# Kernel optimization log

Hardware: AMD Instinct MI355X
Metric: run time of the kernel (lower is better)

## Reference

```python
import jax, jax.numpy as jnp
import numpy as np

B, F, E, U = 16384, 1024, 8, 512
EH1, EH2 = 1024, 1024
TH1, TH2 = 512, 256
T = 4


def setup_inputs() -> dict:
    key = jax.random.key(0)
    ks = jax.random.split(key, 16)
    s = lambda k, shape: jax.random.normal(k, shape, dtype=jnp.float32) * 0.02
    return {
        "x": jax.random.normal(ks[0], (B, F), dtype=jnp.float32),
        # stacked expert MLP params [E, ...]
        "We1": s(ks[1], (E, F, EH1)), "be1": s(ks[2], (E, EH1)),
        "We2": s(ks[3], (E, EH1, EH2)), "be2": s(ks[4], (E, EH2)),
        "We3": s(ks[5], (E, EH2, U)), "be3": s(ks[6], (E, U)),
        # per-task gates [T, F, E]
        "Wg": jax.random.normal(ks[7], (T, F, E), dtype=jnp.float32),
        # stacked tower params [T, ...]
        "Wt1": s(ks[8], (T, U, TH1)), "bt1": s(ks[9], (T, TH1)),
        "Wt2": s(ks[10], (T, TH1, TH2)), "bt2": s(ks[11], (T, TH2)),
        "Wt3": s(ks[12], (T, TH2, 1)), "bt3": s(ks[13], (T, 1)),
    }


def reference(x, We1, be1, We2, be2, We3, be3, Wg, Wt1, bt1, Wt2, bt2, Wt3, bt3):
    relu = jax.nn.relu
    # experts: all E small MLPs batched as one grouped GEMM chain -> [E, B, U]
    h = relu(jnp.einsum('bf,efh->ebh', x, We1) + be1[:, None, :])
    h = relu(jnp.einsum('ebh,ehk->ebk', h, We2) + be2[:, None, :])
    expert_out = jnp.einsum('ebk,eku->ebu', h, We3) + be3[:, None, :]
    # per-task gates: softmax over expert axis -> [T, B, E]
    gates = jax.nn.softmax(jnp.einsum('bf,tfe->tbe', x, Wg), axis=-1)
    # gate-weighted combine over experts -> [T, B, U]
    ti = jnp.einsum('tbe,ebu->tbu', gates, expert_out)
    # per-task towers -> [T, B, 1]
    g = relu(jnp.einsum('tbu,tuh->tbh', ti, Wt1) + bt1[:, None, :])
    g = relu(jnp.einsum('tbh,thk->tbk', g, Wt2) + bt2[:, None, :])
    out = jnp.einsum('tbk,tko->tbo', g, Wt3) + bt3[:, None, :]
    return out  # [T, B, 1], equivalent to list of per-task [B, 1] outputs
```

## Files before the change

### kernel.cpp

```cpp
#include <hip/hip_runtime.h>
#include <hip/hip_bf16.h>
#include <cstdint>

#define B_ 16384
#define F_ 1024
#define E_ 8
#define U_ 512
#define EH1_ 1024
#define EH2_ 1024
#define TH1_ 512
#define TH2_ 256
#define T_ 4

typedef __attribute__((ext_vector_type(4))) float f32x4;
typedef __attribute__((ext_vector_type(8))) short bf16x8;
typedef __attribute__((ext_vector_type(4))) short s16x4;

__device__ __forceinline__ short f2bf(float f) {
  union { float f; unsigned u; } v; v.f = f;
  unsigned r = v.u + 0x7fffu + ((v.u >> 16) & 1u);
  return (short)(r >> 16);
}
__device__ __forceinline__ float bf2f(short s) {
  union { unsigned u; float f; } v; v.u = ((unsigned)(unsigned short)s) << 16;
  return v.f;
}

__device__ __forceinline__ void gload16(const void* g, void* l) {
  __builtin_amdgcn_global_load_lds(
      (const __attribute__((address_space(1))) void*)g,
      (__attribute__((address_space(3))) void*)l, 16, 0, 0);
}

__global__ __launch_bounds__(256) void conv_dual(const float* __restrict__ in,
                                                 short* __restrict__ ob,
                                                 short* __restrict__ orr, long n) {
  long i = ((long)blockIdx.x * 256 + threadIdx.x) * 8;
  if (i >= n) return;
  const float4* p = (const float4*)(in + i);
  float4 a = p[0], b = p[1];
  float v[8] = {a.x, a.y, a.z, a.w, b.x, b.y, b.z, b.w};
  bf16x8 o, r;
#pragma unroll
  for (int j = 0; j < 8; j++) {
    short s = f2bf(v[j]);
    o[j] = s;
    r[j] = f2bf(v[j] - bf2f(s));
  }
  *(bf16x8*)(ob + i) = o;
  *(bf16x8*)(orr + i) = r;
}

__global__ __launch_bounds__(256) void trans_conv(const float* __restrict__ W,
                                                  short* __restrict__ Wt, int K, int N) {
  __shared__ float tile[32][33];
  const int e = blockIdx.z;
  const int k0 = blockIdx.x * 32, n0 = blockIdx.y * 32;
  const float* We = W + (size_t)e * K * N;
  short* Wte = Wt + (size_t)e * N * K;
  const int tx = threadIdx.x, ty = threadIdx.y;
#pragma unroll
  for (int r = 0; r < 32; r += 8)
    tile[ty + r][tx] = We[(size_t)(k0 + ty + r) * N + (n0 + tx)];
  __syncthreads();
#pragma unroll
  for (int r = 0; r < 32; r += 8)
    Wte[(size_t)(n0 + ty + r) * K + (k0 + tx)] = f2bf(tile[tx][ty + r]);
}

__global__ __launch_bounds__(256) void trans_wg(const float* __restrict__ Wg,
                                                short* __restrict__ Wp,
                                                short* __restrict__ Wr) {
  int idx = blockIdx.x * 256 + threadIdx.x;
  int p = idx >> 10, f = idx & 1023;
  int t = p >> 3, e = p & 7;
  float w = Wg[((size_t)t * F_ + f) * E_ + e];
  short wb = f2bf(w);
  Wp[idx] = wb;
  Wr[idx] = f2bf(w - bf2f(wb));
}

__global__ __launch_bounds__(256) void glogits(const short* __restrict__ xb,
                                               const short* __restrict__ xr,
                                               const short* __restrict__ Wp,
                                               const short* __restrict__ Wr,
                                               float* __restrict__ gates) {
  const int wid = threadIdx.x >> 6, lane = threadIdx.x & 63;
  const int m0 = blockIdx.x * 64 + wid * 16;
  const int fr = lane & 15, kg = (lane >> 4) * 8;
  f32x4 acc[2];
#pragma unroll
  for (int j = 0; j < 2; j++)
#pragma unroll
    for (int r = 0; r < 4; r++) acc[j][r] = 0.f;

  const short* Aterm[3] = {xb, xb, xr};
  const short* Bterm[3] = {Wp, Wr, Wp};
#pragma unroll
  for (int term = 0; term < 3; ++term) {
    const short* A = Aterm[term] + (size_t)(m0 + fr) * F_ + kg;
    const short* Bt0 = Bterm[term] + (size_t)fr * F_ + kg;
    const short* Bt1 = Bterm[term] + (size_t)(16 + fr) * F_ + kg;
    for (int k0 = 0; k0 < F_; k0 += 32) {
      bf16x8 a = *(const bf16x8*)(A + k0);
      bf16x8 b0 = *(const bf16x8*)(Bt0 + k0);
      bf16x8 b1 = *(const bf16x8*)(Bt1 + k0);
      acc[0] = __builtin_amdgcn_mfma_f32_16x16x32_bf16(a, b0, acc[0], 0, 0, 0);
      acc[1] = __builtin_amdgcn_mfma_f32_16x16x32_bf16(a, b1, acc[1], 0, 0, 0);
    }
  }
  const int cc = lane & 15;
#pragma unroll
  for (int j = 0; j < 2; ++j) {
    const int t = j * 2 + (cc >> 3), e = cc & 7;
#pragma unroll
    for (int r = 0; r < 4; ++r) {
      float s = acc[j][r];
      float mx = s;
      mx = fmaxf(mx, __shfl_xor(mx, 1, 64));
      mx = fmaxf(mx, __shfl_xor(mx, 2, 64));
      mx = fmaxf(mx, __shfl_xor(mx, 4, 64));
      float ex = __expf(s - mx);
      float sm = ex;
      sm += __shfl_xor(sm, 1, 64);
      sm += __shfl_xor(sm, 2, 64);
      sm += __shfl_xor(sm, 4, 64);
      const int b = m0 + (lane >> 4) * 4 + r;
      gates[((size_t)t * B_ + b) * E_ + e] = ex / sm;
    }
  }
}

template <int RELU>
__global__ __launch_bounds__(256, 2) void gemm_bt(const short* __restrict__ A0, size_t sA,
                                                  const short* __restrict__ B0, size_t sB,
                                                  const float* __restrict__ bias0, size_t sBias,
                                                  short* __restrict__ C0, size_t sC,
                                                  int M, int N, int K) {
  const int z = blockIdx.z;
  const short* A = A0 + (size_t)z * sA;
  const short* Bt = B0 + (size_t)z * sB;
  const float* bias = bias0 + (size_t)z * sBias;
  short* C = C0 + (size_t)z * sC;

  __shared__ short As[128 * 64];
  __shared__ short Bs[128 * 64];
  const int tid = threadIdx.x;
  const int wid = tid >> 6;
  const int lane = tid & 63;
  const int m0 = blockIdx.x * 128;
  const int n0 = blockIdx.y * 128;
  const int wm = (wid >> 1) * 64;
  const int wn = (wid & 1) * 64;

  f32x4 acc[4][4];
#pragma unroll
  for (int i = 0; i < 4; i++)
#pragma unroll
    for (int j = 0; j < 4; j++)
#pragma unroll
      for (int r = 0; r < 4; r++) acc[i][j][r] = 0.f;

  const int srow8 = lane >> 3;
  const int scolb = (((lane & 7) ^ srow8) << 4);
  const short* aS = A + (size_t)(m0 + wid * 8 + srow8) * K + (scolb >> 1);
  const short* bS = Bt + (size_t)(n0 + wid * 8 + srow8) * K + (scolb >> 1);
  char* Adst = (char*)As + wid * 1024;
  char* Bdst = (char*)Bs + wid * 1024;

  const int fr = lane & 15;
  const int g = lane >> 4;
  const int swzR = (fr & 7) << 4;
  const char* Ard = (const char*)As + (wm + fr) * 128;
  const char* Brd = (const char*)Bs + (wn + fr) * 128;

  for (int k0 = 0; k0 < K; k0 += 64) {
#pragma unroll
    for (int c = 0; c < 4; ++c) {
      gload16(aS + (size_t)c * 32 * K + k0, Adst + c * 4096);
      gload16(bS + (size_t)c * 32 * K + k0, Bdst + c * 4096);
    }
    __syncthreads();
    {
      const int ca = (g * 16) ^ swzR;
      bf16x8 af[4], bfv[4];
#pragma unroll
      for (int i = 0; i < 4; i++) af[i] = *(const bf16x8*)(Ard + i * 2048 + ca);
#pragma unroll
      for (int j = 0; j < 4; j++) bfv[j] = *(const bf16x8*)(Brd + j * 2048 + ca);
      __builtin_amdgcn_s_setprio(1);
#pragma unroll
      for (int i = 0; i < 4; i++)
#pragma unroll
        for (int j = 0; j < 4; j++)
          acc[i][j] = __builtin_amdgcn_mfma_f32_16x16x32_bf16(af[i], bfv[j], acc[i][j], 0, 0, 0);
      __builtin_amdgcn_s_setprio(0);
    }
    {
      const int ca = (64 + g * 16) ^ swzR;
      bf16x8 af[4], bfv[4];
#pragma unroll
      for (int i = 0; i < 4; i++) af[i] = *(const bf16x8*)(Ard + i * 2048 + ca);
#pragma unroll
      for (int j = 0; j < 4; j++) bfv[j] = *(const bf16x8*)(Brd + j * 2048 + ca);
      __builtin_amdgcn_s_setprio(1);
#pragma unroll
      for (int i = 0; i < 4; i++)
#pragma unroll
        for (int j = 0; j < 4; j++)
          acc[i][j] = __builtin_amdgcn_mfma_f32_16x16x32_bf16(af[i], bfv[j], acc[i][j], 0, 0, 0);
      __builtin_amdgcn_s_setprio(0);
    }
    __syncthreads();
  }

  const int cr4 = (lane >> 4) * 4;
  const int cc = lane & 15;
#pragma unroll
  for (int j = 0; j < 4; j++) {
    const int col = n0 + wn + j * 16 + cc;
    const float bv = bias[col];
#pragma unroll
    for (int i = 0; i < 4; i++) {
      const int row = m0 + wm + i * 16 + cr4;
#pragma unroll
      for (int r = 0; r < 4; r++) {
        float v = acc[i][j][r] + bv;
        if (RELU) v = fmaxf(v, 0.f);
        C[(size_t)(row + r) * N + col] = f2bf(v);
      }
    }
  }
}

__global__ __launch_bounds__(256) void combine_kernel(const short* __restrict__ EO,
                                                      const float* __restrict__ gates,
                                                      short* __restrict__ ti,
                                                      int Bc, int b0) {
  const int idx = blockIdx.x * 256 + threadIdx.x;
  const int lb = idx >> 6;
  const int uc = (idx & 63) * 8;
  float acc[T_][8];
#pragma unroll
  for (int t = 0; t < T_; t++)
#pragma unroll
    for (int j = 0; j < 8; j++) acc[t][j] = 0.f;
#pragma unroll
  for (int e = 0; e < E_; e++) {
    bf16x8 v = *(const bf16x8*)&EO[((size_t)e * Bc + lb) * U_ + uc];
    float f[8];
#pragma unroll
    for (int j = 0; j < 8; j++) f[j] = bf2f(v[j]);
#pragma unroll
    for (int t = 0; t < T_; t++) {
      const float g = gates[((size_t)t * B_ + b0 + lb) * E_ + e];
#pragma unroll
      for (int j = 0; j < 8; j++) acc[t][j] += g * f[j];
    }
  }
#pragma unroll
  for (int t = 0; t < T_; t++) {
    bf16x8 o;
#pragma unroll
    for (int j = 0; j < 8; j++) o[j] = f2bf(acc[t][j]);
    *(bf16x8*)&ti[((size_t)t * Bc + lb) * U_ + uc] = o;
  }
}

__global__ __launch_bounds__(256) void tower3_kernel(const short* __restrict__ G2,
                                                     const float* __restrict__ Wt3,
                                                     const float* __restrict__ bt3,
                                                     float* __restrict__ out,
                                                     int bcShift, int b0) {
  const int wid = threadIdx.x >> 6, lane = threadIdx.x & 63;
  const int rowl = blockIdx.x * 4 + wid;
  const int t = rowl >> bcShift;
  const int lb = rowl & ((1 << bcShift) - 1);
  const short* g = G2 + (size_t)rowl * TH2_;
  s16x4 gv = *(const s16x4*)(g + lane * 4);
  float4 wv = *(const float4*)(Wt3 + t * TH2_ + lane * 4);
  float s = bf2f(gv[0]) * wv.x + bf2f(gv[1]) * wv.y + bf2f(gv[2]) * wv.z + bf2f(gv[3]) * wv.w;
#pragma unroll
  for (int off = 32; off; off >>= 1) s += __shfl_xor(s, off, 64);
  if (lane == 0) out[(size_t)t * B_ + b0 + lb] = s + bt3[t];
}

extern "C" void kernel_launch(void* const* d_in, const int* in_sizes, int n_in,
                              void* d_out, int out_size, void* d_ws, size_t ws_size,
                              hipStream_t stream) {
  const float* x   = (const float*)d_in[0];
  const float* We1 = (const float*)d_in[1];
  const float* be1 = (const float*)d_in[2];
  const float* We2 = (const float*)d_in[3];
  const float* be2 = (const float*)d_in[4];
  const float* We3 = (const float*)d_in[5];
  const float* be3 = (const float*)d_in[6];
  const float* Wg  = (const float*)d_in[7];
  const float* Wt1 = (const float*)d_in[8];
  const float* bt1 = (const float*)d_in[9];
  const float* Wt2 = (const float*)d_in[10];
  const float* bt2 = (const float*)d_in[11];
  const float* Wt3 = (const float*)d_in[12];
  const float* bt3 = (const float*)d_in[13];
  float* out = (float*)d_out;
  (void)in_sizes; (void)n_in; (void)out_size;

  char* ws = (char*)d_ws;
  size_t off = 0;
  auto alloc = [&](size_t bytes) {
    char* p = ws + off;
    off += (bytes + 255) & ~(size_t)255;
    return p;
  };
  short* We1b  = (short*)alloc((size_t)E_ * F_ * EH1_ * 2);
  short* We2b  = (short*)alloc((size_t)E_ * EH1_ * EH2_ * 2);
  short* We3b  = (short*)alloc((size_t)E_ * EH2_ * U_ * 2);
  short* Wt1b  = (short*)alloc((size_t)T_ * U_ * TH1_ * 2);
  short* Wt2b  = (short*)alloc((size_t)T_ * TH1_ * TH2_ * 2);
  short* Wgp   = (short*)alloc((size_t)32 * F_ * 2);
  short* Wgr   = (short*)alloc((size_t)32 * F_ * 2);
  float* gates = (float*)alloc((size_t)T_ * B_ * E_ * 4);
  short* xb    = (short*)alloc((size_t)B_ * F_ * 2);
  short* xrb   = (short*)alloc((size_t)B_ * F_ * 2);
  const size_t persist = off;

  int Bc = 16384;
  while (Bc > 256 && persist + (size_t)Bc * 32768 + 65536 > ws_size) Bc >>= 1;
  const int bcShift = __builtin_ctz((unsigned)Bc);

  short* h1 = (short*)alloc((size_t)E_ * Bc * EH1_ * 2);
  short* h2 = (short*)alloc((size_t)E_ * Bc * EH2_ * 2);
  short* EO = h1;
  short* ti = h2;
  short* G1 = h2 + (size_t)Bc * 2048;
  short* G2 = h2 + (size_t)Bc * 4096;

  conv_dual<<<(B_ * F_ / 8 + 255) / 256, 256, 0, stream>>>(x, xb, xrb, (long)B_ * F_);
  dim3 tb(32, 8);
  trans_conv<<<dim3(F_ / 32, EH1_ / 32, E_), tb, 0, stream>>>(We1, We1b, F_, EH1_);
  trans_conv<<<dim3(EH1_ / 32, EH2_ / 32, E_), tb, 0, stream>>>(We2, We2b, EH1_, EH2_);
  trans_conv<<<dim3(EH2_ / 32, U_ / 32, E_), tb, 0, stream>>>(We3, We3b, EH2_, U_);
  trans_conv<<<dim3(U_ / 32, TH1_ / 32, T_), tb, 0, stream>>>(Wt1, Wt1b, U_, TH1_);
  trans_conv<<<dim3(TH1_ / 32, TH2_ / 32, T_), tb, 0, stream>>>(Wt2, Wt2b, TH1_, TH2_);
  trans_wg<<<(32 * F_) / 256, 256, 0, stream>>>(Wg, Wgp, Wgr);

  glogits<<<B_ / 64, 256, 0, stream>>>(xb, xrb, Wgp, Wgr, gates);

  for (int b0 = 0; b0 < B_; b0 += Bc) {
    const short* xc = xb + (size_t)b0 * F_;
    gemm_bt<1><<<dim3(Bc / 128, EH1_ / 128, E_), 256, 0, stream>>>(
        xc, 0, We1b, (size_t)F_ * EH1_, be1, EH1_, h1, (size_t)Bc * EH1_, Bc, EH1_, F_);
    gemm_bt<1><<<dim3(Bc / 128, EH2_ / 128, E_), 256, 0, stream>>>(
        h1, (size_t)Bc * EH1_, We2b, (size_t)EH1_ * EH2_, be2, EH2_, h2, (size_t)Bc * EH2_,
        Bc, EH2_, EH1_);
    gemm_bt<0><<<dim3(Bc / 128, U_ / 128, E_), 256, 0, stream>>>(
        h2, (size_t)Bc * EH2_, We3b, (size_t)EH2_ * U_, be3, U_, EO, (size_t)Bc * U_,
        Bc, U_, EH2_);
    combine_kernel<<<(Bc * 64) / 256, 256, 0, stream>>>(EO, gates, ti, Bc, b0);
    gemm_bt<1><<<dim3(Bc / 128, TH1_ / 128, T_), 256, 0, stream>>>(
        ti, (size_t)Bc * U_, Wt1b, (size_t)U_ * TH1_, bt1, TH1_, G1, (size_t)Bc * TH1_,
        Bc, TH1_, U_);
    gemm_bt<1><<<dim3(Bc / 128, TH2_ / 128, T_), 256, 0, stream>>>(
        G1, (size_t)Bc * TH1_, Wt2b, (size_t)TH1_ * TH2_, bt2, TH2_, G2, (size_t)Bc * TH2_,
        Bc, TH2_, TH1_);
    tower3_kernel<<<T_ * Bc / 4, 256, 0, stream>>>(G2, Wt3, bt3, out, bcShift, b0);
  }
}
```

Baseline: 977.7 us.

## Double-buffer LDS tiles in bf16 GEMM to overlap global loads with MFMA

Converts the GEMM main loop from single-buffered LDS staging to a two-stage ping-pong pipeline. Tile k+2 is loaded into the buffer just consumed while MFMAs run on registers already read. Manual vmcnt/lgkmcnt waits plus barriers replace the two __syncthreads per iteration. This doubles LDS use to 64KB per block, which may limit occupancy to the stated 2 blocks per CU, and it issues redundant clamped loads on the last iterations.

```diff
diff --git a/kernel.cpp b/kernel.cpp
--- a/kernel.cpp
+++ b/kernel.cpp
@@ -143,8 +143,8 @@
   const float* bias = bias0 + (size_t)z * sBias;
   short* C = C0 + (size_t)z * sC;
 
-  __shared__ short As[128 * 64];
-  __shared__ short Bs[128 * 64];
+  __shared__ short As[2][128 * 64];
+  __shared__ short Bs[2][128 * 64];
   const int tid = threadIdx.x;
   const int wid = tid >> 6;
   const int lane = tid & 63;
@@ -165,53 +165,68 @@
   const int scolb = (((lane & 7) ^ srow8) << 4);
   const short* aS = A + (size_t)(m0 + wid * 8 + srow8) * K + (scolb >> 1);
   const short* bS = Bt + (size_t)(n0 + wid * 8 + srow8) * K + (scolb >> 1);
-  char* Adst = (char*)As + wid * 1024;
-  char* Bdst = (char*)Bs + wid * 1024;
+
+  auto stage = [&](int buf, int k0) {
+#pragma unroll
+    for (int c = 0; c < 4; ++c) {
+      gload16(aS + (size_t)c * 32 * K + k0, (char*)As + buf * 16384 + wid * 1024 + c * 4096);
+      gload16(bS + (size_t)c * 32 * K + k0, (char*)Bs + buf * 16384 + wid * 1024 + c * 4096);
+    }
+  };
 
   const int fr = lane & 15;
   const int g = lane >> 4;
   const int swzR = (fr & 7) << 4;
-  const char* Ard = (const char*)As + (wm + fr) * 128;
-  const char* Brd = (const char*)Bs + (wn + fr) * 128;
-
-  for (int k0 = 0; k0 < K; k0 += 64) {
-#pragma unroll
-    for (int c = 0; c < 4; ++c) {
-      gload16(aS + (size_t)c * 32 * K + k0, Adst + c * 4096);
-      gload16(bS + (size_t)c * 32 * K + k0, Bdst + c * 4096);
-    }
-    __syncthreads();
-    {
-      const int ca = (g * 16) ^ swzR;
-      bf16x8 af[4], bfv[4];
-#pragma unroll
-      for (int i = 0; i < 4; i++) af[i] = *(const bf16x8*)(Ard + i * 2048 + ca);
-#pragma unroll
-      for (int j = 0; j < 4; j++) bfv[j] = *(const bf16x8*)(Brd + j * 2048 + ca);
-      __builtin_amdgcn_s_setprio(1);
-#pragma unroll
-      for (int i = 0; i < 4; i++)
-#pragma unroll
-        for (int j = 0; j < 4; j++)
-          acc[i][j] = __builtin_amdgcn_mfma_f32_16x16x32_bf16(af[i], bfv[j], acc[i][j], 0, 0, 0);
-      __builtin_amdgcn_s_setprio(0);
-    }
-    {
-      const int ca = (64 + g * 16) ^ swzR;
-      bf16x8 af[4], bfv[4];
-#pragma unroll
-      for (int i = 0; i < 4; i++) af[i] = *(const bf16x8*)(Ard + i * 2048 + ca);
-#pragma unroll
-      for (int j = 0; j < 4; j++) bfv[j] = *(const bf16x8*)(Brd + j * 2048 + ca);
-      __builtin_amdgcn_s_setprio(1);
-#pragma unroll
-      for (int i = 0; i < 4; i++)
-#pragma unroll
-        for (int j = 0; j < 4; j++)
-          acc[i][j] = __builtin_amdgcn_mfma_f32_16x16x32_bf16(af[i], bfv[j], acc[i][j], 0, 0, 0);
-      __builtin_amdgcn_s_setprio(0);
-    }
-    __syncthreads();
+  const int rdA = (wm + fr) * 128;
+  const int rdB = (wn + fr) * 128;
+  const int ca0 = (g * 16) ^ swzR;
+  const int ca1 = (64 + g * 16) ^ swzR;
+
+  const int NT = K >> 6;
+
+  stage(0, 0);
+  stage(1, (NT > 1 ? 64 : 0));
+  asm volatile("s_waitcnt vmcnt(8)" ::: "memory");
+  __builtin_amdgcn_sched_barrier(0);
+  __builtin_amdgcn_s_barrier();
+
+  for (int t = 0; t < NT; ++t) {
+    const int cur = t & 1;
+    const char* Ab = (const char*)As + cur * 16384;
+    const char* Bb = (const char*)Bs + cur * 16384;
+    bf16x8 a0[4], b0[4], a1[4], b1[4];
+#pragma unroll
+    for (int i = 0; i < 4; i++) {
+      a0[i] = *(const bf16x8*)(Ab + rdA + i * 2048 + ca0);
+      a1[i] = *(const bf16x8*)(Ab + rdA + i * 2048 + ca1);
+      b0[i] = *(const bf16x8*)(Bb + rdB + i * 2048 + ca0);
+      b1[i] = *(const bf16x8*)(Bb + rdB + i * 2048 + ca1);
+    }
+    asm volatile("s_waitcnt lgkmcnt(0)" ::: "memory");
+    __builtin_amdgcn_sched_barrier(0);
+    __builtin_amdgcn_s_barrier();
+    __builtin_amdgcn_sched_barrier(0);
+
+    const int k2 = (t + 2 < NT ? t + 2 : NT - 1) * 64;
+    stage(cur, k2);
+
+    __builtin_amdgcn_s_setprio(1);
+#pragma unroll
+    for (int i = 0; i < 4; i++)
+#pragma unroll
+      for (int j = 0; j < 4; j++)
+        acc[i][j] = __builtin_amdgcn_mfma_f32_16x16x32_bf16(a0[i], b0[j], acc[i][j], 0, 0, 0);
+#pragma unroll
+    for (int i = 0; i < 4; i++)
+#pragma unroll
+      for (int j = 0; j < 4; j++)
+        acc[i][j] = __builtin_amdgcn_mfma_f32_16x16x32_bf16(a1[i], b1[j], acc[i][j], 0, 0, 0);
+    __builtin_amdgcn_s_setprio(0);
+
+    asm volatile("s_waitcnt vmcnt(8)" ::: "memory");
+    __builtin_amdgcn_sched_barrier(0);
+    __builtin_amdgcn_s_barrier();
+    __builtin_amdgcn_sched_barrier(0);
   }
 
   const int cr4 = (lane >> 4) * 4;
```

After: 996.9 us. About the same (+2.0%).

## Add 256x256-tile pipelined GEMM kernel for expert MLP layers

Applied to the files above, without the earlier changes.

Introduces a new 512-thread GEMM kernel with 256x256 output tiles, 128KB of double-buffered LDS filled by direct global-to-LDS loads, XOR swizzling, interleaved load/MFMA phases separated by barriers with raised MFMA priority, and an XCD-aware block remapping. The three expert GEMMs switch to this kernel to get more data reuse per tile and better overlap of memory and compute. In exchange it uses heavy register and LDS pressure, which limits occupancy, and it assumes M, N and K are multiples of the tile sizes.

```diff
diff --git a/kernel.cpp b/kernel.cpp
--- a/kernel.cpp
+++ b/kernel.cpp
@@ -31,6 +31,8 @@
       (const __attribute__((address_space(1))) void*)g,
       (__attribute__((address_space(3))) void*)l, 16, 0, 0);
 }
+
+#define PHFENCE() __builtin_amdgcn_sched_barrier(0)
 
 __global__ __launch_bounds__(256) void conv_dual(const float* __restrict__ in,
                                                  short* __restrict__ ob,
@@ -129,6 +131,162 @@
       gates[((size_t)t * B_ + b) * E_ + e] = ex / sm;
     }
   }
+}
+
+template <int RELU>
+__global__ __launch_bounds__(512, 2) void gemm256(const short* __restrict__ A0, size_t sA,
+                                                  const short* __restrict__ B0, size_t sB,
+                                                  const float* __restrict__ bias0, size_t sBias,
+                                                  short* __restrict__ C0, size_t sC,
+                                                  int M, int N, int K) {
+  unsigned nwg = gridDim.x * gridDim.y * gridDim.z;
+  unsigned lid = (blockIdx.z * gridDim.y + blockIdx.y) * gridDim.x + blockIdx.x;
+  unsigned sid = (nwg & 7u) ? lid : (lid & 7u) * (nwg >> 3) + (lid >> 3);
+  const int bx = sid % gridDim.x;
+  unsigned rem = sid / gridDim.x;
+  const int by = rem % gridDim.y;
+  const int bz = rem / gridDim.y;
+
+  const short* A = A0 + (size_t)bz * sA;
+  const short* Bt = B0 + (size_t)bz * sB;
+  const float* bias = bias0 + (size_t)bz * sBias;
+  short* C = C0 + (size_t)bz * sC;
+
+  __shared__ char lds[131072];
+  const int tid = threadIdx.x;
+  const int wid = tid >> 6, lane = tid & 63;
+  const int wr = wid >> 2, wc = wid & 3;
+  const int m0g = bx * 256, n0g = by * 256;
+
+  f32x4 acc[8][4];
+#pragma unroll
+  for (int m = 0; m < 8; m++)
+#pragma unroll
+    for (int n = 0; n < 4; n++)
+#pragma unroll
+      for (int r = 0; r < 4; r++) acc[m][n][r] = 0.f;
+
+  const int trow = tid >> 3;
+  const int tcolsh = (((tid & 7) ^ (trow & 7)) << 3);
+  const short* aRow = A + (size_t)(m0g + trow) * K + tcolsh;
+  const short* bRow = Bt + (size_t)(n0g + trow) * K + tcolsh;
+  const int wpart = wid << 10;
+
+  auto stA = [&](int buf, int u, int kt) {
+#pragma unroll
+    for (int c = 0; c < 2; ++c)
+      gload16(aRow + (size_t)(u * 64 + c * 128) * K + kt * 64,
+              lds + buf * 32768 + u * 8192 + c * 16384 + wpart);
+  };
+  auto stB = [&](int buf, int u, int kt) {
+#pragma unroll
+    for (int c = 0; c < 2; ++c)
+      gload16(bRow + (size_t)(u * 128 + c * 64) * K + kt * 64,
+              lds + 65536 + buf * 32768 + u * 16384 + c * 8192 + wpart);
+  };
+
+  const int fr = lane & 15, g = lane >> 4;
+  const int swz = (fr & 7) << 4;
+  const int rdA = (wr * 128 + fr) * 128;
+  const int rdB = (wc * 64 + fr) * 128;
+  const int ca0 = (g * 16) ^ swz;
+  const int ca1 = (64 + g * 16) ^ swz;
+
+  auto ldA = [&](int buf, int m, int ca) -> bf16x8 {
+    return *(const bf16x8*)(lds + buf * 32768 + rdA + m * 2048 + ca);
+  };
+  auto ldB = [&](int buf, int n, int ca) -> bf16x8 {
+    return *(const bf16x8*)(lds + 65536 + buf * 32768 + rdB + n * 2048 + ca);
+  };
+
+  const int NT = K >> 6, NI = NT >> 1;
+
+  stA(0, 0, 0); stB(0, 0, 0); stA(0, 1, 0); stB(0, 1, 0);
+  stA(1, 0, 1); stB(1, 0, 1);
+  asm volatile("s_waitcnt vmcnt(4)" ::: "memory");
+  PHFENCE(); __builtin_amdgcn_s_barrier(); PHFENCE();
+
+  bf16x8 a[4], b0[4], b1[4];
+#define MFMA16(ACCB, BV)                                                          \
+  __builtin_amdgcn_s_setprio(1);                                                  \
+  _Pragma("unroll") for (int m = 0; m < 4; ++m)                                   \
+      _Pragma("unroll") for (int n = 0; n < 4; ++n)                               \
+          acc[ACCB + m][n] =                                                      \
+              __builtin_amdgcn_mfma_f32_16x16x32_bf16(a[m], BV[n], acc[ACCB + m][n], 0, 0, 0); \
+  __builtin_amdgcn_s_setprio(0);
+#define BAR() PHFENCE(); __builtin_amdgcn_s_barrier(); PHFENCE();
+
+  for (int i = 0; i < NI; ++i) {
+    const int tO = 2 * i + 1;
+    const int tE2 = (2 * i + 2 < NT) ? 2 * i + 2 : NT - 2;
+    const int tO2 = (2 * i + 3 < NT) ? 2 * i + 3 : NT - 1;
+
+#pragma unroll
+    for (int m = 0; m < 4; ++m) a[m] = ldA(0, m, ca0);
+#pragma unroll
+    for (int n = 0; n < 4; ++n) b0[n] = ldB(0, n, ca0);
+    stB(1, 1, tO);
+    BAR(); MFMA16(0, b0); BAR();
+#pragma unroll
+    for (int m = 0; m < 4; ++m) a[m] = ldA(0, m, ca1);
+#pragma unroll
+    for (int n = 0; n < 4; ++n) b1[n] = ldB(0, n, ca1);
+    stA(1, 1, tO);
+    BAR(); MFMA16(0, b1); BAR();
+#pragma unroll
+    for (int m = 0; m < 4; ++m) a[m] = ldA(0, 4 + m, ca0);
+    stA(0, 0, tE2);
+    BAR(); MFMA16(4, b0); BAR();
+#pragma unroll
+    for (int m = 0; m < 4; ++m) a[m] = ldA(0, 4 + m, ca1);
+    stB(0, 0, tE2);
+    BAR(); MFMA16(4, b1);
+    asm volatile("s_waitcnt vmcnt(4)" ::: "memory");
+    BAR();
+#pragma unroll
+    for (int m = 0; m < 4; ++m) a[m] = ldA(1, m, ca0);
+#pragma unroll
+    for (int n = 0; n < 4; ++n) b0[n] = ldB(1, n, ca0);
+    stB(0, 1, tE2);
+    BAR(); MFMA16(0, b0); BAR();
+#pragma unroll
+    for (int m = 0; m < 4; ++m) a[m] = ldA(1, m, ca1);
+#pragma unroll
+    for (int n = 0; n < 4; ++n) b1[n] = ldB(1, n, ca1);
+    stA(0, 1, tE2);
+    BAR(); MFMA16(0, b1); BAR();
+#pragma unroll
+    for (int m = 0; m < 4; ++m) a[m] = ldA(1, 4 + m, ca0);
+    stA(1, 0, tO2);
+    BAR(); MFMA16(4, b0); BAR();
+#pragma unroll
+    for (int m = 0; m < 4; ++m) a[m] = ldA(1, 4 + m, ca1);
+    stB(1, 0, tO2);
+    BAR(); MFMA16(4, b1);
+    asm volatile("s_waitcnt vmcnt(4)" ::: "memory");
+    BAR();
+  }
+  asm volatile("s_waitcnt vmcnt(0)" ::: "memory");
+
+  const int cr4 = (lane >> 4) * 4;
+  const int cc = lane & 15;
+#pragma unroll
+  for (int j = 0; j < 4; ++j) {
+    const int col = n0g + wc * 64 + j * 16 + cc;
+    const float bv = bias[col];
+#pragma unroll
+    for (int m = 0; m < 8; ++m) {
+      const int row = m0g + wr * 128 + m * 16 + cr4;
+#pragma unroll
+      for (int r = 0; r < 4; ++r) {
+        float v = acc[m][j][r] + bv;
+        if (RELU) v = fmaxf(v, 0.f);
+        C[(size_t)(row + r) * N + col] = f2bf(v);
+      }
+    }
+  }
+#undef MFMA16
+#undef BAR
 }
 
 template <int RELU>
@@ -348,12 +506,12 @@
 
   for (int b0 = 0; b0 < B_; b0 += Bc) {
     const short* xc = xb + (size_t)b0 * F_;
-    gemm_bt<1><<<dim3(Bc / 128, EH1_ / 128, E_), 256, 0, stream>>>(
+    gemm256<1><<<dim3(Bc / 256, EH1_ / 256, E_), 512, 0, stream>>>(
         xc, 0, We1b, (size_t)F_ * EH1_, be1, EH1_, h1, (size_t)Bc * EH1_, Bc, EH1_, F_);
-    gemm_bt<1><<<dim3(Bc / 128, EH2_ / 128, E_), 256, 0, stream>>>(
+    gemm256<1><<<dim3(Bc / 256, EH2_ / 256, E_), 512, 0, stream>>>(
         h1, (size_t)Bc * EH1_, We2b, (size_t)EH1_ * EH2_, be2, EH2_, h2, (size_t)Bc * EH2_,
         Bc, EH2_, EH1_);
-    gemm_bt<0><<<dim3(Bc / 128, U_ / 128, E_), 256, 0, stream>>>(
+    gemm256<0><<<dim3(Bc / 256, U_ / 256, E_), 512, 0, stream>>>(
         h2, (size_t)Bc * EH2_, We3b, (size_t)EH2_ * U_, be3, U_, EO, (size_t)Bc * U_,
         Bc, U_, EH2_);
     combine_kernel<<<(Bc * 64) / 256, 256, 0, stream>>>(EO, gates, ti, Bc, b0);
```

Measured after the change: 1.042 ms. 1.07x slower.
